# Performance work log

Measured on AMD Instinct MI355X. Metric: run time of the kernel, lower is better.

Reference implementation:

```python
import jax, jax.numpy as jnp
import numpy as np

L = 16            # num_levels
F = 2             # features per level
T = 1 << 19       # hashmap size
BASE = 16         # base resolution
RES = 512         # desired_resolution (outer trilinear grid)
N_PTS = 262144

# 8 corner offsets of a unit cube, [8,3]
OFFS = np.array([[(c >> 0) & 1, (c >> 1) & 1, (c >> 2) & 1] for c in range(8)], dtype=np.uint32)
OFFS_J = jnp.asarray(OFFS)
OFFS_B = jnp.asarray(OFFS.astype(bool))
P1 = jnp.uint32(2654435761)
P2 = jnp.uint32(805459861)


def hash_encode(x01, table):
    """Instant-NGP multiresolution hash encoding. x01: [N,3] in [0,1]. table: [L,T,F]."""
    feats = []
    for l in range(L):
        res = BASE * (2 ** l)
        pos = x01 * res                      # [N,3]
        p0 = jnp.floor(pos)
        frac = pos - p0                      # [N,3]
        corners = p0.astype(jnp.uint32)[:, None, :] + OFFS_J[None]   # [N,8,3]
        if (res + 1) ** 3 <= T:              # dense level
            c = jnp.minimum(corners, jnp.uint32(res))
            idx = c[..., 0] + c[..., 1] * jnp.uint32(res + 1) + c[..., 2] * jnp.uint32((res + 1) * (res + 1))
        else:                                # hashed level (spatial hash, xor of primes)
            idx = corners[..., 0] ^ (corners[..., 1] * P1) ^ (corners[..., 2] * P2)
            idx = idx & jnp.uint32(T - 1)
        g = table[l][idx.astype(jnp.int32)]  # [N,8,F]
        w = jnp.where(OFFS_B[None], frac[:, None, :], 1.0 - frac[:, None, :]).prod(-1)  # [N,8]
        feats.append(jnp.einsum('nc,ncf->nf', w, g))
    return jnp.concatenate(feats, axis=-1)   # [N, L*F]


def mlp(x, W0, W1, W2):
    h = jax.nn.relu(x @ W0)
    h = jax.nn.relu(h @ W1)
    return h @ W2


def setup_inputs() -> dict:
    key = jax.random.key(0)
    k1, k2, k3, k4, k5 = jax.random.split(key, 5)
    xyz = jax.random.uniform(k1, (N_PTS, 3), dtype=jnp.float32, minval=-1.0, maxval=1.0)
    table = jax.random.uniform(k2, (L, T, F), dtype=jnp.float32, minval=-1e-4, maxval=1e-4)
    W0 = jax.random.normal(k3, (L * F, 64), dtype=jnp.float32) * (1.0 / np.sqrt(L * F))
    W1 = jax.random.normal(k4, (64, 64), dtype=jnp.float32) * (1.0 / 8.0)
    W2 = jax.random.normal(k5, (64, 8), dtype=jnp.float32) * (1.0 / 8.0)
    return {"xyz": xyz, "table": table, "W0": W0, "W1": W1, "W2": W2, "bound": 1}


def reference(xyz, table, W0, W1, W2, bound):
    xn = (xyz + bound) / (2 * bound)          # [N,3] in [0,1]
    coords = xn * RES
    c0 = jnp.clip(jnp.floor(coords), 0.0, RES - 1.0)   # [N,3] floats holding ints
    frac = coords - c0                         # u,v,w per-axis [N,3]
    out = jnp.zeros((xyz.shape[0], 8), dtype=xyz.dtype)
    for b in range(8):
        bits = np.array([(b >> 0) & 1, (b >> 1) & 1, (b >> 2) & 1], dtype=np.float32)
        cc = (c0 + bits) / RES                 # corner point normalized to [0,1]
        f = mlp(hash_encode(cc, table), W0, W1, W2)   # [N,8]
        w = jnp.where(bits.astype(bool), frac, 1.0 - frac).prod(-1)  # [N]
        out = out + w[:, None] * f
    return out
```

## Files before the change

kernel.cpp:

```cpp
#include <hip/hip_runtime.h>


typedef __attribute__((ext_vector_type(8))) short short8_t;
typedef __attribute__((ext_vector_type(4))) float f32x4;

static constexpr unsigned kT    = 1u << 19;
static constexpr unsigned kMask = kT - 1u;
static constexpr unsigned cP1   = 2654435761u;
static constexpr unsigned cP2   = 805459861u;
static constexpr int      BLOCK = 256;
static constexpr int      TOFF  = 4096;
static constexpr unsigned DOFF  = 1u << 21;
static constexpr unsigned DN0   = 4913;
static constexpr unsigned DN1   = 40850;
static constexpr unsigned DENSE_N = 315475;
static constexpr unsigned PARTO = 2621440u;
static constexpr size_t   WS_NEED  = ((size_t)TOFF + (1u << 21)) * 4;
static constexpr size_t   WS_NEED2 = ((size_t)PARTO + (1u << 22)) * 4;

static __device__ __forceinline__ unsigned bf16_rn(float x) {
    unsigned u = __float_as_uint(x);
    return (u + 0x7fffu + ((u >> 16) & 1u)) >> 16;
}

static __device__ __forceinline__ float2 bf2dec(unsigned u) {
    return make_float2(__uint_as_float(u << 16),
                       __uint_as_float(u & 0xffff0000u));
}

static __device__ __forceinline__ unsigned cvtpk(float lo, float hi) {
    unsigned r;
    asm("v_cvt_pk_bf16_f32 %0, %1, %2" : "=v"(r) : "v"(lo), "v"(hi));
    return r;
}

static __device__ __forceinline__ f32x4 mfma16(short8_t a, short8_t b, f32x4 c) {
    return __builtin_amdgcn_mfma_f32_16x16x32_bf16(a, b, c, 0, 0, 0);
}

__global__ __launch_bounds__(256)
void prep_all(const float* __restrict__ W0, const float* __restrict__ W1,
              const float* __restrict__ W2, const float2* __restrict__ tbl,
              unsigned* __restrict__ ws, int ncc, int ncf, int ncd)
{
    const int bx = blockIdx.x, tid = threadIdx.x;
    if (bx < ncc) {
        const int i = bx * 256 + tid;
        const float4 v = ((const float4*)(tbl + (size_t)3 * kT))[i];
        ((uint2*)(ws + TOFF))[i] =
            make_uint2(bf16_rn(v.x) | (bf16_rn(v.y) << 16),
                       bf16_rn(v.z) | (bf16_rn(v.w) << 16));
    } else if (bx < ncc + ncf) {
        const int i = (bx - ncc) * 256 + tid;
        const unsigned vv = (1u << 20) - 1u - (unsigned)i;
        const int s = __clz((int)vv) - 12;
        const unsigned fo = (1u << 20) - ((1u << 20) >> s);
        const unsigned j = (unsigned)i - fo;
        const float2 e = tbl[((size_t)(5 + s) << 19) + ((size_t)j << s)];
        (ws + TOFF + (1u << 20))[i] = bf16_rn(e.x) | (bf16_rn(e.y) << 16);
    } else if (bx < ncc + ncf + ncd) {
        const int i = (bx - ncc - ncf) * 256 + tid;
        if (i < (int)DENSE_N) {
            int l, off;
            if (i < (int)DN0)      { l = 0; off = i; }
            else if (i < (int)DN1) { l = 1; off = i - (int)DN0; }
            else                   { l = 2; off = i - (int)DN1; }
            const float2 e = tbl[(size_t)l * kT + off];
            ws[TOFF + DOFF + i] = bf16_rn(e.x) | (bf16_rn(e.y) << 16);
        }
    } else {
        const int t = (bx - ncc - ncf - ncd) * 4 + (tid >> 6);
        if (t >= 14) return;
        const int lane = tid & 63;
        const int n = lane & 15, q = lane >> 4;
        unsigned hi[4];
        #pragma unroll
        for (int d = 0; d < 4; ++d) {
            unsigned h2[2];
            #pragma unroll
            for (int s = 0; s < 2; ++s) {
                const int j = d * 2 + s;
                float v;
                if (t < 4) {
                    v = W0[(q * 8 + j) * 64 + t * 16 + n];
                } else {
                    const int kp = (j < 4) ? (q * 4 + j) : (16 + q * 4 + (j - 4));
                    if (t < 12) v = W1[(((t - 4) & 1) * 32 + kp) * 64 + ((t - 4) >> 1) * 16 + n];
                    else        v = (n < 8) ? W2[((t - 12) * 32 + kp) * 8 + n] : 0.0f;
                }
                h2[s] = bf16_rn(v);
            }
            hi[d] = h2[0] | (h2[1] << 16);
        }
        ((uint4*)ws)[t * 64 + lane] = make_uint4(hi[0], hi[1], hi[2], hi[3]);
    }
}

__global__ __launch_bounds__(256, 8)
void ngp_pa(const float* __restrict__ xyz, const int* __restrict__ boundp,
            unsigned* __restrict__ ws)
{
    const int tid = threadIdx.x;
    const int ge  = blockIdx.x * 256 + tid;
    const int pt  = ge >> 3;
    const int b   = ge & 7;

    const float bnd = (float)boundp[0];
    const float sc  = 0.5f / bnd;
    const float cxf = (xyz[pt * 3 + 0] + bnd) * sc * 512.0f;
    const float cyf = (xyz[pt * 3 + 1] + bnd) * sc * 512.0f;
    const float czf = (xyz[pt * 3 + 2] + bnd) * sc * 512.0f;
    const float c0x = fminf(fmaxf(floorf(cxf), 0.0f), 511.0f);
    const float c0y = fminf(fmaxf(floorf(cyf), 0.0f), 511.0f);
    const float c0z = fminf(fmaxf(floorf(czf), 0.0f), 511.0f);
    const unsigned kx = (unsigned)c0x + (unsigned)(b & 1);
    const unsigned ky = (unsigned)c0y + (unsigned)((b >> 1) & 1);
    const unsigned kz = (unsigned)c0z + (unsigned)((b >> 2) & 1);

    const unsigned* __restrict__ tbx = ws + TOFF;
    unsigned gH[2][8];
    #pragma unroll
    for (int l = 3; l < 5; ++l) {
        const int d = 5 - l;
        const unsigned qx = kx >> d, qy = ky >> d, qz = kz >> d;
        const unsigned hy0 = qy * cP1, hy1 = hy0 + cP1;
        const unsigned hz0 = qz * cP2, hz1 = hz0 + cP2;
        const unsigned x1u = qx + 1u;
        unsigned hidx[8];
        hidx[0] = (qx  ^ hy0 ^ hz0) & kMask;  hidx[1] = (x1u ^ hy0 ^ hz0) & kMask;
        hidx[2] = (qx  ^ hy1 ^ hz0) & kMask;  hidx[3] = (x1u ^ hy1 ^ hz0) & kMask;
        hidx[4] = (qx  ^ hy0 ^ hz1) & kMask;  hidx[5] = (x1u ^ hy0 ^ hz1) & kMask;
        hidx[6] = (qx  ^ hy1 ^ hz1) & kMask;  hidx[7] = (x1u ^ hy1 ^ hz1) & kMask;
        const unsigned* __restrict__ base = tbx + (size_t)(l - 3) * kT;
        #pragma unroll
        for (int c = 0; c < 8; ++c) gH[l - 3][c] = base[hidx[c]];
    }

    unsigned xd34[2];
    #pragma unroll
    for (int l = 3; l < 5; ++l) {
        const int d = 5 - l;
        const unsigned m = (1u << d) - 1u;
        const float inv = 1.0f / (float)(1 << d);
        const float fx = (float)(kx & m) * inv;
        const float fy = (float)(ky & m) * inv;
        const float fz = (float)(kz & m) * inv;
        const float2 g0 = bf2dec(gH[l - 3][0]), g1 = bf2dec(gH[l - 3][1]);
        const float2 g2 = bf2dec(gH[l - 3][2]), g3 = bf2dec(gH[l - 3][3]);
        const float2 g4 = bf2dec(gH[l - 3][4]), g5 = bf2dec(gH[l - 3][5]);
        const float2 g6 = bf2dec(gH[l - 3][6]), g7 = bf2dec(gH[l - 3][7]);
        const float wx1 = fx, wx0 = 1.0f - fx;
        const float wy1 = fy, wy0 = 1.0f - fy;
        const float wz1 = fz, wz0 = 1.0f - fz;
        const float w00 = wx0 * wy0, w10 = wx1 * wy0, w01 = wx0 * wy1, w11 = wx1 * wy1;
        const float a0 = w00 * wz0, a1 = w10 * wz0, a2 = w01 * wz0, a3 = w11 * wz0;
        const float a4 = w00 * wz1, a5 = w10 * wz1, a6 = w01 * wz1, a7 = w11 * wz1;
        const float vx = a0 * g0.x + a1 * g1.x + a2 * g2.x + a3 * g3.x
                       + a4 * g4.x + a5 * g5.x + a6 * g6.x + a7 * g7.x;
        const float vy = a0 * g0.y + a1 * g1.y + a2 * g2.y + a3 * g3.y
                       + a4 * g4.y + a5 * g5.y + a6 * g6.y + a7 * g7.y;
        xd34[l - 3] = cvtpk(vx, vy);
    }
    ((uint2*)(ws + PARTO))[ge] = make_uint2(xd34[0], xd34[1]);
}

__global__ __launch_bounds__(BLOCK, 5)
void ngp_pb(const float*  __restrict__ xyz,
            const int*    __restrict__ boundp,
            const unsigned* __restrict__ wsw,
            float*        __restrict__ out)
{
    __shared__ __align__(16) unsigned lds[4096];
    const int tid  = threadIdx.x;
    const int lane = tid & 63;
    const int wv   = tid >> 6;
    const int col  = lane & 15;
    const int q    = lane >> 4;
    const int swz  = (tid ^ (tid >> 2) ^ (tid >> 4)) & 3;

    const unsigned* __restrict__ tbx = wsw + TOFF;
    const float bnd = (float)boundp[0];
    const float sc  = 0.5f / bnd;
    const f32x4 zero = {0.0f, 0.0f, 0.0f, 0.0f};

    const int ge = blockIdx.x * BLOCK + tid;
    const int pt = ge >> 3;
    const int b  = ge & 7;

    const float cxf = (xyz[pt * 3 + 0] + bnd) * sc * 512.0f;
    const float cyf = (xyz[pt * 3 + 1] + bnd) * sc * 512.0f;
    const float czf = (xyz[pt * 3 + 2] + bnd) * sc * 512.0f;
    const float c0x = fminf(fmaxf(floorf(cxf), 0.0f), 511.0f);
    const float c0y = fminf(fmaxf(floorf(cyf), 0.0f), 511.0f);
    const float c0z = fminf(fmaxf(floorf(czf), 0.0f), 511.0f);
    const float frx = cxf - c0x;
    const float fry = cyf - c0y;
    const float frz = czf - c0z;

    const unsigned kx = (unsigned)c0x + (unsigned)(b & 1);
    const unsigned ky = (unsigned)c0y + (unsigned)((b >> 1) & 1);
    const unsigned kz = (unsigned)c0z + (unsigned)((b >> 2) & 1);

    const float wb = ((b & 1) ? frx : 1.0f - frx)
                   * ((b & 2) ? fry : 1.0f - fry)
                   * ((b & 4) ? frz : 1.0f - frz);

    const unsigned kyp = ky * cP1;
    const unsigned kzp = kz * cP2;
    const unsigned X   = kx ^ kyp ^ kzp;
    unsigned gfu[11];
    #pragma unroll
    for (int l = 5; l < 16; ++l) {
        const int s = l - 5;
        const unsigned base = (1u << 20) + ((1u << 20) - ((1u << 20) >> s));
        gfu[l - 5] = tbx[base + (X & (kMask >> s))];
    }

    const uint2 p34 = ((const uint2*)(wsw + PARTO))[ge];

    unsigned xd[16];
    #pragma unroll
    for (int l = 0; l < 3; ++l) {
        const int d = 5 - l;
        const unsigned m = (1u << d) - 1u;
        const float inv = 1.0f / (float)(1 << d);
        const unsigned qx = kx >> d, qy = ky >> d, qz = kz >> d;
        const float fx = (float)(kx & m) * inv;
        const float fy = (float)(ky & m) * inv;
        const float fz = (float)(kz & m) * inv;
        const unsigned res = 16u << l;
        const unsigned R = res + 1u, R2 = R * R;
        const unsigned x0 = (qx < res ? qx : res);
        const unsigned x1 = (qx + 1u < res ? qx + 1u : res);
        const unsigned y0 = (qy < res ? qy : res) * R;
        const unsigned y1 = (qy + 1u < res ? qy + 1u : res) * R;
        const unsigned z0 = (qz < res ? qz : res) * R2;
        const unsigned z1 = (qz + 1u < res ? qz + 1u : res) * R2;
        const unsigned dbase = DOFF + (l == 0 ? 0u : (l == 1 ? DN0 : DN1));
        const unsigned* __restrict__ base = tbx + dbase;
        const float2 g0 = bf2dec(base[x0 + y0 + z0]), g1 = bf2dec(base[x1 + y0 + z0]);
        const float2 g2 = bf2dec(base[x0 + y1 + z0]), g3 = bf2dec(base[x1 + y1 + z0]);
        const float2 g4 = bf2dec(base[x0 + y0 + z1]), g5 = bf2dec(base[x1 + y0 + z1]);
        const float2 g6 = bf2dec(base[x0 + y1 + z1]), g7 = bf2dec(base[x1 + y1 + z1]);
        const float wx1 = fx, wx0 = 1.0f - fx;
        const float wy1 = fy, wy0 = 1.0f - fy;
        const float wz1 = fz, wz0 = 1.0f - fz;
        const float w00 = wx0 * wy0, w10 = wx1 * wy0, w01 = wx0 * wy1, w11 = wx1 * wy1;
        const float a0 = w00 * wz0, a1 = w10 * wz0, a2 = w01 * wz0, a3 = w11 * wz0;
        const float a4 = w00 * wz1, a5 = w10 * wz1, a6 = w01 * wz1, a7 = w11 * wz1;
        const float vx = a0 * g0.x + a1 * g1.x + a2 * g2.x + a3 * g3.x
                       + a4 * g4.x + a5 * g5.x + a6 * g6.x + a7 * g7.x;
        const float vy = a0 * g0.y + a1 * g1.y + a2 * g2.y + a3 * g3.y
                       + a4 * g4.y + a5 * g5.y + a6 * g6.y + a7 * g7.y;
        xd[l] = cvtpk(vx, vy);
    }
    xd[3] = p34.x;
    xd[4] = p34.y;
    #pragma unroll
    for (int l = 5; l < 16; ++l) xd[l] = gfu[l - 5];

    {
        uint4* xrow = (uint4*)(lds + tid * 16);
        xrow[swz]     = make_uint4(xd[0],  xd[1],  xd[2],  xd[3]);
        xrow[swz ^ 1] = make_uint4(xd[4],  xd[5],  xd[6],  xd[7]);
        xrow[swz ^ 2] = make_uint4(xd[8],  xd[9],  xd[10], xd[11]);
        xrow[swz ^ 3] = make_uint4(xd[12], xd[13], xd[14], xd[15]);
    }

    asm volatile("s_waitcnt lgkmcnt(0)" ::: "memory");
    __builtin_amdgcn_sched_barrier(0);

    short8_t w[14];
    {
        const short8_t* __restrict__ wfr = (const short8_t*)wsw;
        #pragma unroll
        for (int t = 0; t < 14; ++t) w[t] = wfr[t * 64 + lane];
    }

    #pragma unroll 1
    for (int g = 0; g < 4; ++g) {
        const int ev  = wv * 64 + g * 16 + col;
        const int esw = ((ev ^ (ev >> 2) ^ (ev >> 4)) & 3) ^ q;
        const short8_t xb = *(const short8_t*)(lds + ev * 16 + esw * 4);
        const float wbv = __shfl(wb, g * 16 + col, 64);

        unsigned hp0[4], hp1[4];
        #pragma unroll
        for (int mt = 0; mt < 4; ++mt) {
            f32x4 a = mfma16(w[mt], xb, zero);
            hp0[mt] = cvtpk(fmaxf(a[0], 0.0f), fmaxf(a[1], 0.0f));
            hp1[mt] = cvtpk(fmaxf(a[2], 0.0f), fmaxf(a[3], 0.0f));
        }
        uint4 u0 = make_uint4(hp0[0], hp1[0], hp0[1], hp1[1]);
        uint4 u1 = make_uint4(hp0[2], hp1[2], hp0[3], hp1[3]);
        short8_t bk0 = *(short8_t*)&u0;
        short8_t bk1 = *(short8_t*)&u1;

        #pragma unroll
        for (int mt = 0; mt < 4; ++mt) {
            f32x4 a = mfma16(w[4 + mt * 2], bk0, zero);
            a = mfma16(w[5 + mt * 2], bk1, a);
            hp0[mt] = cvtpk(fmaxf(a[0], 0.0f), fmaxf(a[1], 0.0f));
            hp1[mt] = cvtpk(fmaxf(a[2], 0.0f), fmaxf(a[3], 0.0f));
        }
        u0 = make_uint4(hp0[0], hp1[0], hp0[1], hp1[1]);
        u1 = make_uint4(hp0[2], hp1[2], hp0[3], hp1[3]);
        bk0 = *(short8_t*)&u0;
        bk1 = *(short8_t*)&u1;

        f32x4 a3 = mfma16(w[12], bk0, zero);
        a3 = mfma16(w[13], bk1, a3);

        float v0 = wbv * a3[0], v1 = wbv * a3[1], v2 = wbv * a3[2], v3 = wbv * a3[3];
        #pragma unroll
        for (int s = 1; s < 8; s <<= 1) {
            v0 += __shfl_xor(v0, s);
            v1 += __shfl_xor(v1, s);
            v2 += __shfl_xor(v2, s);
            v3 += __shfl_xor(v3, s);
        }
        if (((lane & 7) == 0) && q < 2) {
            const int p = (blockIdx.x * BLOCK + ev) >> 3;
            *(float4*)(out + p * 8 + q * 4) = make_float4(v0, v1, v2, v3);
        }
    }
}

template<bool BT>
__global__ __launch_bounds__(BLOCK, 5)
void ngp_mfma(const float*  __restrict__ xyz,
              const float2* __restrict__ tbl,
              const int*    __restrict__ boundp,
              const unsigned* __restrict__ wsw,
              float*        __restrict__ out,
              int ntiles)
{
    __shared__ __align__(16) unsigned lds[4096];
    const int tid  = threadIdx.x;
    const int lane = tid & 63;
    const int wv   = tid >> 6;
    const int col  = lane & 15;
    const int q    = lane >> 4;
    const int swz  = (tid ^ (tid >> 2) ^ (tid >> 4)) & 3;

    const unsigned* __restrict__ tbx = wsw + TOFF;
    const float bnd = (float)boundp[0];
    const float sc  = 0.5f / bnd;
    const f32x4 zero = {0.0f, 0.0f, 0.0f, 0.0f};

    const int ge = blockIdx.x * BLOCK + tid;
    const int pt = ge >> 3;
    const int b  = ge & 7;

    const float cxf = (xyz[pt * 3 + 0] + bnd) * sc * 512.0f;
    const float cyf = (xyz[pt * 3 + 1] + bnd) * sc * 512.0f;
    const float czf = (xyz[pt * 3 + 2] + bnd) * sc * 512.0f;
    const float c0x = fminf(fmaxf(floorf(cxf), 0.0f), 511.0f);
    const float c0y = fminf(fmaxf(floorf(cyf), 0.0f), 511.0f);
    const float c0z = fminf(fmaxf(floorf(czf), 0.0f), 511.0f);
    const float frx = cxf - c0x;
    const float fry = cyf - c0y;
    const float frz = czf - c0z;

    const unsigned kx = (unsigned)c0x + (unsigned)(b & 1);
    const unsigned ky = (unsigned)c0y + (unsigned)((b >> 1) & 1);
    const unsigned kz = (unsigned)c0z + (unsigned)((b >> 2) & 1);

    const float wb = ((b & 1) ? frx : 1.0f - frx)
                   * ((b & 2) ? fry : 1.0f - fry)
                   * ((b & 4) ? frz : 1.0f - frz);

    const unsigned kyp = ky * cP1;
    const unsigned kzp = kz * cP2;
    const unsigned X   = kx ^ kyp ^ kzp;
    unsigned gfu[11];
    float2   gff[11];
    #pragma unroll
    for (int l = 5; l < 16; ++l) {
        const int s = l - 5;
        if (BT) {
            const unsigned base = (1u << 20) + ((1u << 20) - ((1u << 20) >> s));
            gfu[l - 5] = tbx[base + (X & (kMask >> s))];
        } else {
            const unsigned idx = ((kx << s) ^ (kyp << s) ^ (kzp << s)) & kMask;
            gff[l - 5] = tbl[(size_t)l * kT + idx];
        }
    }

    unsigned gH[2][8];
    float2   gHf[2][8];
    #pragma unroll
    for (int l = 3; l < 5; ++l) {
        const int d = 5 - l;
        const unsigned qx = kx >> d, qy = ky >> d, qz = kz >> d;
        const unsigned hy0 = qy * cP1, hy1 = hy0 + cP1;
        const unsigned hz0 = qz * cP2, hz1 = hz0 + cP2;
        const unsigned x1u = qx + 1u;
        unsigned hidx[8];
        hidx[0] = (qx  ^ hy0 ^ hz0) & kMask;  hidx[1] = (x1u ^ hy0 ^ hz0) & kMask;
        hidx[2] = (qx  ^ hy1 ^ hz0) & kMask;  hidx[3] = (x1u ^ hy1 ^ hz0) & kMask;
        hidx[4] = (qx  ^ hy0 ^ hz1) & kMask;  hidx[5] = (x1u ^ hy0 ^ hz1) & kMask;
        hidx[6] = (qx  ^ hy1 ^ hz1) & kMask;  hidx[7] = (x1u ^ hy1 ^ hz1) & kMask;
        if (BT) {
            const unsigned* __restrict__ base = tbx + (size_t)(l - 3) * kT;
            #pragma unroll
            for (int c = 0; c < 8; ++c) gH[l - 3][c] = base[hidx[c]];
        } else {
            const float2* __restrict__ base = tbl + (size_t)l * kT;
            #pragma unroll
            for (int c = 0; c < 8; ++c) gHf[l - 3][c] = base[hidx[c]];
        }
    }

    float2 gc[5];
    #pragma unroll
    for (int l = 0; l < 5; ++l) {
        const int d = 5 - l;
        const unsigned m = (1u << d) - 1u;
        const float inv = 1.0f / (float)(1 << d);
        const unsigned qx = kx >> d, qy = ky >> d, qz = kz >> d;
        const float fx = (float)(kx & m) * inv;
        const float fy = (float)(ky & m) * inv;
        const float fz = (float)(kz & m) * inv;
        float2 g0, g1, g2, g3, g4, g5, g6, g7;
        if (l < 3) {
            const unsigned res = 16u << l;
            const unsigned R = res + 1u, R2 = R * R;
            const unsigned x0 = (qx < res ? qx : res);
            const unsigned x1 = (qx + 1u < res ? qx + 1u : res);
            const unsigned y0 = (qy < res ? qy : res) * R;
            const unsigned y1 = (qy + 1u < res ? qy + 1u : res) * R;
            const unsigned z0 = (qz < res ? qz : res) * R2;
            const unsigned z1 = (qz + 1u < res ? qz + 1u : res) * R2;
            const float2* __restrict__ base = tbl + (size_t)l * kT;
            g0 = base[x0 + y0 + z0]; g1 = base[x1 + y0 + z0];
            g2 = base[x0 + y1 + z0]; g3 = base[x1 + y1 + z0];
            g4 = base[x0 + y0 + z1]; g5 = base[x1 + y0 + z1];
            g6 = base[x0 + y1 + z1]; g7 = base[x1 + y1 + z1];
        } else if (BT) {
            g0 = bf2dec(gH[l - 3][0]); g1 = bf2dec(gH[l - 3][1]);
            g2 = bf2dec(gH[l - 3][2]); g3 = bf2dec(gH[l - 3][3]);
            g4 = bf2dec(gH[l - 3][4]); g5 = bf2dec(gH[l - 3][5]);
            g6 = bf2dec(gH[l - 3][6]); g7 = bf2dec(gH[l - 3][7]);
        } else {
            g0 = gHf[l - 3][0]; g1 = gHf[l - 3][1]; g2 = gHf[l - 3][2]; g3 = gHf[l - 3][3];
            g4 = gHf[l - 3][4]; g5 = gHf[l - 3][5]; g6 = gHf[l - 3][6]; g7 = gHf[l - 3][7];
        }
        const float wx1 = fx, wx0 = 1.0f - fx;
        const float wy1 = fy, wy0 = 1.0f - fy;
        const float wz1 = fz, wz0 = 1.0f - fz;
        const float w00 = wx0 * wy0, w10 = wx1 * wy0, w01 = wx0 * wy1, w11 = wx1 * wy1;
        const float a0 = w00 * wz0, a1 = w10 * wz0, a2 = w01 * wz0, a3 = w11 * wz0;
        const float a4 = w00 * wz1, a5 = w10 * wz1, a6 = w01 * wz1, a7 = w11 * wz1;
        float vx = a0 * g0.x + a1 * g1.x + a2 * g2.x + a3 * g3.x
                 + a4 * g4.x + a5 * g5.x + a6 * g6.x + a7 * g7.x;
        float vy = a0 * g0.y + a1 * g1.y + a2 * g2.y + a3 * g3.y
                 + a4 * g4.y + a5 * g5.y + a6 * g6.y + a7 * g7.y;
        gc[l] = make_float2(vx, vy);
    }

    unsigned xd[16];
    #pragma unroll
    for (int l = 0; l < 5; ++l)
        xd[l] = cvtpk(gc[l].x, gc[l].y);
    #pragma unroll
    for (int l = 5; l < 16; ++l) {
        if (BT) xd[l] = gfu[l - 5];
        else    xd[l] = cvtpk(gff[l - 5].x, gff[l - 5].y);
    }
    {
        uint4* xrow = (uint4*)(lds + tid * 16);
        xrow[swz]     = make_uint4(xd[0],  xd[1],  xd[2],  xd[3]);
        xrow[swz ^ 1] = make_uint4(xd[4],  xd[5],  xd[6],  xd[7]);
        xrow[swz ^ 2] = make_uint4(xd[8],  xd[9],  xd[10], xd[11]);
        xrow[swz ^ 3] = make_uint4(xd[12], xd[13], xd[14], xd[15]);
    }

    asm volatile("s_waitcnt lgkmcnt(0)" ::: "memory");
    __builtin_amdgcn_sched_barrier(0);

    short8_t w[14];
    {
        const short8_t* __restrict__ wfr = (const short8_t*)wsw;
        #pragma unroll
        for (int t = 0; t < 14; ++t) w[t] = wfr[t * 64 + lane];
    }

    #pragma unroll 1
    for (int g = 0; g < 4; ++g) {
        const int ev  = wv * 64 + g * 16 + col;
        const int esw = ((ev ^ (ev >> 2) ^ (ev >> 4)) & 3) ^ q;
        const short8_t xb = *(const short8_t*)(lds + ev * 16 + esw * 4);
        const float wbv = __shfl(wb, g * 16 + col, 64);

        unsigned hp0[4], hp1[4];
        #pragma unroll
        for (int mt = 0; mt < 4; ++mt) {
            f32x4 a = mfma16(w[mt], xb, zero);
            hp0[mt] = cvtpk(fmaxf(a[0], 0.0f), fmaxf(a[1], 0.0f));
            hp1[mt] = cvtpk(fmaxf(a[2], 0.0f), fmaxf(a[3], 0.0f));
        }
        uint4 u0 = make_uint4(hp0[0], hp1[0], hp0[1], hp1[1]);
        uint4 u1 = make_uint4(hp0[2], hp1[2], hp0[3], hp1[3]);
        short8_t bk0 = *(short8_t*)&u0;
        short8_t bk1 = *(short8_t*)&u1;

        #pragma unroll
        for (int mt = 0; mt < 4; ++mt) {
            f32x4 a = mfma16(w[4 + mt * 2], bk0, zero);
            a = mfma16(w[5 + mt * 2], bk1, a);
            hp0[mt] = cvtpk(fmaxf(a[0], 0.0f), fmaxf(a[1], 0.0f));
            hp1[mt] = cvtpk(fmaxf(a[2], 0.0f), fmaxf(a[3], 0.0f));
        }
        u0 = make_uint4(hp0[0], hp1[0], hp0[1], hp1[1]);
        u1 = make_uint4(hp0[2], hp1[2], hp0[3], hp1[3]);
        bk0 = *(short8_t*)&u0;
        bk1 = *(short8_t*)&u1;

        f32x4 a3 = mfma16(w[12], bk0, zero);
        a3 = mfma16(w[13], bk1, a3);

        float v0 = wbv * a3[0], v1 = wbv * a3[1], v2 = wbv * a3[2], v3 = wbv * a3[3];
        #pragma unroll
        for (int s = 1; s < 8; s <<= 1) {
            v0 += __shfl_xor(v0, s);
            v1 += __shfl_xor(v1, s);
            v2 += __shfl_xor(v2, s);
            v3 += __shfl_xor(v3, s);
        }
        if (((lane & 7) == 0) && q < 2) {
            const int p = (blockIdx.x * BLOCK + ev) >> 3;
            *(float4*)(out + p * 8 + q * 4) = make_float4(v0, v1, v2, v3);
        }
    }
}

extern "C" void kernel_launch(void* const* d_in, const int* in_sizes, int n_in,
                              void* d_out, int out_size, void* d_ws, size_t ws_size,
                              hipStream_t stream) {
    const float*  xyz = (const float*)d_in[0];
    const float2* tbl = (const float2*)d_in[1];
    const float*  W0  = (const float*)d_in[2];
    const float*  W1  = (const float*)d_in[3];
    const float*  W2  = (const float*)d_in[4];
    const int*    bnd = (const int*)d_in[5];
    float* out = (float*)d_out;

    const int npts   = in_sizes[0] / 3;
    const int total  = npts * 8;
    const int ntiles = total / BLOCK;

    const bool big2 = (ws_size >= WS_NEED2);
    const bool big  = (ws_size >= WS_NEED);
    const int ncc = big ? (1 << 19) / 256 : 0;
    const int ncf = big ? ((1 << 20) - (1 << 9)) / 256 : 0;
    const int ncd = big2 ? (int)((DENSE_N + 255) / 256) : 0;

    hipLaunchKernelGGL(prep_all, dim3(ncc + ncf + ncd + 4), dim3(256), 0, stream,
                       W0, W1, W2, tbl, (unsigned*)d_ws, ncc, ncf, ncd);

    if (big2) {
        hipLaunchKernelGGL(ngp_pa, dim3(total / 256), dim3(256), 0, stream,
                           xyz, bnd, (unsigned*)d_ws);
        hipLaunchKernelGGL(ngp_pb, dim3(ntiles), dim3(BLOCK), 0, stream,
                           xyz, bnd, (const unsigned*)d_ws, out);
    } else if (big) {
        hipLaunchKernelGGL(ngp_mfma<true>, dim3(ntiles), dim3(BLOCK), 0, stream,
                           xyz, tbl, bnd, (const unsigned*)d_ws, out, ntiles);
    } else {
        hipLaunchKernelGGL(ngp_mfma<false>, dim3(ntiles), dim3(BLOCK), 0, stream,
                           xyz, tbl, bnd, (const unsigned*)d_ws, out, ntiles);
    }
}
```

Before: 214.5 us.

## Fold dense levels 0-1 into one upsampled grid and use nontemporal memory ops

Precomputes level-0 features on the level-1 (33^3) grid. Every corner coordinate is even on the level-1 lattice, so the level-0 trilinear result can be stored next to the level-1 value in one 8-byte entry. Level 0 then needs no gathers of its own, cutting the dense-level gather count in the main kernel from 24 to 16. Separately, many table loads and stores switch to nontemporal builtins and ngp_pb's launch bound rises to 8 waves. This adds a prep pass with an extra rounding stage of level-0 features to bf16, and risks register spills at the higher occupancy target.

```diff
diff --git a/kernel.cpp b/kernel.cpp
--- a/kernel.cpp
+++ b/kernel.cpp
@@ -3,6 +3,7 @@
 
 typedef __attribute__((ext_vector_type(8))) short short8_t;
 typedef __attribute__((ext_vector_type(4))) float f32x4;
+typedef unsigned long long ull;
 
 static constexpr unsigned kT    = 1u << 19;
 static constexpr unsigned kMask = kT - 1u;
@@ -10,10 +11,10 @@
 static constexpr unsigned cP2   = 805459861u;
 static constexpr int      BLOCK = 256;
 static constexpr int      TOFF  = 4096;
-static constexpr unsigned DOFF  = 1u << 21;
-static constexpr unsigned DN0   = 4913;
-static constexpr unsigned DN1   = 40850;
-static constexpr unsigned DENSE_N = 315475;
+static constexpr unsigned D01   = 1u << 21;
+static constexpr unsigned N01   = 35937u;
+static constexpr unsigned D2    = D01 + 72000u;
+static constexpr unsigned N2    = 274625u;
 static constexpr unsigned PARTO = 2621440u;
 static constexpr size_t   WS_NEED  = ((size_t)TOFF + (1u << 21)) * 4;
 static constexpr size_t   WS_NEED2 = ((size_t)PARTO + (1u << 22)) * 4;
@@ -41,35 +42,74 @@
 __global__ __launch_bounds__(256)
 void prep_all(const float* __restrict__ W0, const float* __restrict__ W1,
               const float* __restrict__ W2, const float2* __restrict__ tbl,
-              unsigned* __restrict__ ws, int ncc, int ncf, int ncd)
+              unsigned* __restrict__ ws, int ncc, int ncf, int ncd, int nc01)
 {
     const int bx = blockIdx.x, tid = threadIdx.x;
     if (bx < ncc) {
         const int i = bx * 256 + tid;
-        const float4 v = ((const float4*)(tbl + (size_t)3 * kT))[i];
-        ((uint2*)(ws + TOFF))[i] =
-            make_uint2(bf16_rn(v.x) | (bf16_rn(v.y) << 16),
-                       bf16_rn(v.z) | (bf16_rn(v.w) << 16));
+        const ull* __restrict__ p = (const ull*)(tbl + (size_t)3 * kT);
+        const ull a = __builtin_nontemporal_load(p + 2 * (size_t)i);
+        const ull b = __builtin_nontemporal_load(p + 2 * (size_t)i + 1);
+        const ull o = (ull)(bf16_rn(__uint_as_float((unsigned)a))
+                          | (bf16_rn(__uint_as_float((unsigned)(a >> 32))) << 16))
+                    | ((ull)(bf16_rn(__uint_as_float((unsigned)b))
+                          | (bf16_rn(__uint_as_float((unsigned)(b >> 32))) << 16)) << 32);
+        __builtin_nontemporal_store(o, (ull*)(ws + TOFF) + i);
     } else if (bx < ncc + ncf) {
         const int i = (bx - ncc) * 256 + tid;
         const unsigned vv = (1u << 20) - 1u - (unsigned)i;
         const int s = __clz((int)vv) - 12;
         const unsigned fo = (1u << 20) - ((1u << 20) >> s);
         const unsigned j = (unsigned)i - fo;
-        const float2 e = tbl[((size_t)(5 + s) << 19) + ((size_t)j << s)];
-        (ws + TOFF + (1u << 20))[i] = bf16_rn(e.x) | (bf16_rn(e.y) << 16);
+        const ull e = __builtin_nontemporal_load(
+            (const ull*)tbl + ((size_t)(5 + s) << 19) + ((size_t)j << s));
+        const unsigned o = bf16_rn(__uint_as_float((unsigned)e))
+                         | (bf16_rn(__uint_as_float((unsigned)(e >> 32))) << 16);
+        __builtin_nontemporal_store(o, ws + TOFF + (1u << 20) + i);
     } else if (bx < ncc + ncf + ncd) {
         const int i = (bx - ncc - ncf) * 256 + tid;
-        if (i < (int)DENSE_N) {
-            int l, off;
-            if (i < (int)DN0)      { l = 0; off = i; }
-            else if (i < (int)DN1) { l = 1; off = i - (int)DN0; }
-            else                   { l = 2; off = i - (int)DN1; }
-            const float2 e = tbl[(size_t)l * kT + off];
-            ws[TOFF + DOFF + i] = bf16_rn(e.x) | (bf16_rn(e.y) << 16);
+        if (i < (int)N2) {
+            const ull e = __builtin_nontemporal_load(
+                (const ull*)tbl + (size_t)2 * kT + i);
+            const unsigned o = bf16_rn(__uint_as_float((unsigned)e))
+                             | (bf16_rn(__uint_as_float((unsigned)(e >> 32))) << 16);
+            __builtin_nontemporal_store(o, ws + TOFF + D2 + i);
+        }
+    } else if (bx < ncc + ncf + ncd + nc01) {
+        const int i = (bx - ncc - ncf - ncd) * 256 + tid;
+        if (i < (int)N01) {
+            const int vz = i / 1089;
+            const int r  = i - vz * 1089;
+            const int vy = r / 33;
+            const int vx = r - vy * 33;
+            const float2 f1 = tbl[(size_t)kT + i];
+            const int x0 = vx >> 1, y0 = vy >> 1, z0 = vz >> 1;
+            const int x1 = (x0 + 1 > 16) ? 16 : x0 + 1;
+            const int y1 = (y0 + 1 > 16) ? 16 : y0 + 1;
+            const int z1 = (z0 + 1 > 16) ? 16 : z0 + 1;
+            const float fx = (vx & 1) ? 0.5f : 0.0f;
+            const float fy = (vy & 1) ? 0.5f : 0.0f;
+            const float fz = (vz & 1) ? 0.5f : 0.0f;
+            const int Y0 = y0 * 17, Y1 = y1 * 17, Z0 = z0 * 289, Z1 = z1 * 289;
+            const float2 g0 = tbl[x0 + Y0 + Z0], g1 = tbl[x1 + Y0 + Z0];
+            const float2 g2 = tbl[x0 + Y1 + Z0], g3 = tbl[x1 + Y1 + Z0];
+            const float2 g4 = tbl[x0 + Y0 + Z1], g5 = tbl[x1 + Y0 + Z1];
+            const float2 g6 = tbl[x0 + Y1 + Z1], g7 = tbl[x1 + Y1 + Z1];
+            const float wx1 = fx, wx0 = 1.0f - fx;
+            const float wy1 = fy, wy0 = 1.0f - fy;
+            const float wz1 = fz, wz0 = 1.0f - fz;
+            const float w00 = wx0 * wy0, w10 = wx1 * wy0, w01 = wx0 * wy1, w11 = wx1 * wy1;
+            const float a0 = w00 * wz0, a1 = w10 * wz0, a2 = w01 * wz0, a3 = w11 * wz0;
+            const float a4 = w00 * wz1, a5 = w10 * wz1, a6 = w01 * wz1, a7 = w11 * wz1;
+            const float f0x = a0 * g0.x + a1 * g1.x + a2 * g2.x + a3 * g3.x
+                            + a4 * g4.x + a5 * g5.x + a6 * g6.x + a7 * g7.x;
+            const float f0y = a0 * g0.y + a1 * g1.y + a2 * g2.y + a3 * g3.y
+                            + a4 * g4.y + a5 * g5.y + a6 * g6.y + a7 * g7.y;
+            const ull o = (ull)cvtpk(f0x, f0y) | ((ull)cvtpk(f1.x, f1.y) << 32);
+            __builtin_nontemporal_store(o, (ull*)(ws + TOFF + D01) + i);
         }
     } else {
-        const int t = (bx - ncc - ncf - ncd) * 4 + (tid >> 6);
+        const int t = (bx - ncc - ncf - ncd - nc01) * 4 + (tid >> 6);
         if (t >= 14) return;
         const int lane = tid & 63;
         const int n = lane & 15, q = lane >> 4;
@@ -107,9 +147,12 @@
 
     const float bnd = (float)boundp[0];
     const float sc  = 0.5f / bnd;
-    const float cxf = (xyz[pt * 3 + 0] + bnd) * sc * 512.0f;
-    const float cyf = (xyz[pt * 3 + 1] + bnd) * sc * 512.0f;
-    const float czf = (xyz[pt * 3 + 2] + bnd) * sc * 512.0f;
+    const float pxv = __builtin_nontemporal_load(xyz + pt * 3 + 0);
+    const float pyv = __builtin_nontemporal_load(xyz + pt * 3 + 1);
+    const float pzv = __builtin_nontemporal_load(xyz + pt * 3 + 2);
+    const float cxf = (pxv + bnd) * sc * 512.0f;
+    const float cyf = (pyv + bnd) * sc * 512.0f;
+    const float czf = (pzv + bnd) * sc * 512.0f;
     const float c0x = fminf(fmaxf(floorf(cxf), 0.0f), 511.0f);
     const float c0y = fminf(fmaxf(floorf(cyf), 0.0f), 511.0f);
     const float c0z = fminf(fmaxf(floorf(czf), 0.0f), 511.0f);
@@ -161,10 +204,11 @@
                        + a4 * g4.y + a5 * g5.y + a6 * g6.y + a7 * g7.y;
         xd34[l - 3] = cvtpk(vx, vy);
     }
-    ((uint2*)(ws + PARTO))[ge] = make_uint2(xd34[0], xd34[1]);
-}
-
-__global__ __launch_bounds__(BLOCK, 5)
+    const ull o = (ull)xd34[0] | ((ull)xd34[1] << 32);
+    __builtin_nontemporal_store(o, (ull*)(ws + PARTO) + ge);
+}
+
+__global__ __launch_bounds__(BLOCK, 8)
 void ngp_pb(const float*  __restrict__ xyz,
             const int*    __restrict__ boundp,
             const unsigned* __restrict__ wsw,
@@ -187,9 +231,12 @@
     const int pt = ge >> 3;
     const int b  = ge & 7;
 
-    const float cxf = (xyz[pt * 3 + 0] + bnd) * sc * 512.0f;
-    const float cyf = (xyz[pt * 3 + 1] + bnd) * sc * 512.0f;
-    const float czf = (xyz[pt * 3 + 2] + bnd) * sc * 512.0f;
+    const float pxv = __builtin_nontemporal_load(xyz + pt * 3 + 0);
+    const float pyv = __builtin_nontemporal_load(xyz + pt * 3 + 1);
+    const float pzv = __builtin_nontemporal_load(xyz + pt * 3 + 2);
+    const float cxf = (pxv + bnd) * sc * 512.0f;
+    const float cyf = (pyv + bnd) * sc * 512.0f;
+    const float czf = (pzv + bnd) * sc * 512.0f;
     const float c0x = fminf(fmaxf(floorf(cxf), 0.0f), 511.0f);
     const float c0y = fminf(fmaxf(floorf(cyf), 0.0f), 511.0f);
     const float c0z = fminf(fmaxf(floorf(czf), 0.0f), 511.0f);
@@ -216,32 +263,62 @@
         gfu[l - 5] = tbx[base + (X & (kMask >> s))];
     }
 
-    const uint2 p34 = ((const uint2*)(wsw + PARTO))[ge];
+    const ull pv = __builtin_nontemporal_load((const ull*)(wsw + PARTO) + ge);
 
     unsigned xd[16];
-    #pragma unroll
-    for (int l = 0; l < 3; ++l) {
-        const int d = 5 - l;
-        const unsigned m = (1u << d) - 1u;
-        const float inv = 1.0f / (float)(1 << d);
-        const unsigned qx = kx >> d, qy = ky >> d, qz = kz >> d;
-        const float fx = (float)(kx & m) * inv;
-        const float fy = (float)(ky & m) * inv;
-        const float fz = (float)(kz & m) * inv;
-        const unsigned res = 16u << l;
-        const unsigned R = res + 1u, R2 = R * R;
-        const unsigned x0 = (qx < res ? qx : res);
-        const unsigned x1 = (qx + 1u < res ? qx + 1u : res);
-        const unsigned y0 = (qy < res ? qy : res) * R;
-        const unsigned y1 = (qy + 1u < res ? qy + 1u : res) * R;
-        const unsigned z0 = (qz < res ? qz : res) * R2;
-        const unsigned z1 = (qz + 1u < res ? qz + 1u : res) * R2;
-        const unsigned dbase = DOFF + (l == 0 ? 0u : (l == 1 ? DN0 : DN1));
-        const unsigned* __restrict__ base = tbx + dbase;
-        const float2 g0 = bf2dec(base[x0 + y0 + z0]), g1 = bf2dec(base[x1 + y0 + z0]);
-        const float2 g2 = bf2dec(base[x0 + y1 + z0]), g3 = bf2dec(base[x1 + y1 + z0]);
-        const float2 g4 = bf2dec(base[x0 + y0 + z1]), g5 = bf2dec(base[x1 + y0 + z1]);
-        const float2 g6 = bf2dec(base[x0 + y1 + z1]), g7 = bf2dec(base[x1 + y1 + z1]);
+    {
+        const unsigned qx = kx >> 4, qy = ky >> 4, qz = kz >> 4;
+        const float fx = (float)(kx & 15u) * 0.0625f;
+        const float fy = (float)(ky & 15u) * 0.0625f;
+        const float fz = (float)(kz & 15u) * 0.0625f;
+        const unsigned x0 = qx, x1 = (qx + 1u > 32u) ? 32u : qx + 1u;
+        const unsigned y0 = qy * 33u, y1 = ((qy + 1u > 32u) ? 32u : qy + 1u) * 33u;
+        const unsigned z0 = qz * 1089u, z1 = ((qz + 1u > 32u) ? 32u : qz + 1u) * 1089u;
+        const uint2* __restrict__ b01 = (const uint2*)(tbx + D01);
+        const uint2 h0 = b01[x0 + y0 + z0], h1 = b01[x1 + y0 + z0];
+        const uint2 h2 = b01[x0 + y1 + z0], h3 = b01[x1 + y1 + z0];
+        const uint2 h4 = b01[x0 + y0 + z1], h5 = b01[x1 + y0 + z1];
+        const uint2 h6 = b01[x0 + y1 + z1], h7 = b01[x1 + y1 + z1];
+        const float wx1 = fx, wx0 = 1.0f - fx;
+        const float wy1 = fy, wy0 = 1.0f - fy;
+        const float wz1 = fz, wz0 = 1.0f - fz;
+        const float w00 = wx0 * wy0, w10 = wx1 * wy0, w01 = wx0 * wy1, w11 = wx1 * wy1;
+        const float a0 = w00 * wz0, a1 = w10 * wz0, a2 = w01 * wz0, a3 = w11 * wz0;
+        const float a4 = w00 * wz1, a5 = w10 * wz1, a6 = w01 * wz1, a7 = w11 * wz1;
+        float f0x, f0y, f1x, f1y;
+        float2 d;
+        d = bf2dec(h0.x); f0x  = a0 * d.x; f0y  = a0 * d.y;
+        d = bf2dec(h0.y); f1x  = a0 * d.x; f1y  = a0 * d.y;
+        d = bf2dec(h1.x); f0x += a1 * d.x; f0y += a1 * d.y;
+        d = bf2dec(h1.y); f1x += a1 * d.x; f1y += a1 * d.y;
+        d = bf2dec(h2.x); f0x += a2 * d.x; f0y += a2 * d.y;
+        d = bf2dec(h2.y); f1x += a2 * d.x; f1y += a2 * d.y;
+        d = bf2dec(h3.x); f0x += a3 * d.x; f0y += a3 * d.y;
+        d = bf2dec(h3.y); f1x += a3 * d.x; f1y += a3 * d.y;
+        d = bf2dec(h4.x); f0x += a4 * d.x; f0y += a4 * d.y;
+        d = bf2dec(h4.y); f1x += a4 * d.x; f1y += a4 * d.y;
+        d = bf2dec(h5.x); f0x += a5 * d.x; f0y += a5 * d.y;
+        d = bf2dec(h5.y); f1x += a5 * d.x; f1y += a5 * d.y;
+        d = bf2dec(h6.x); f0x += a6 * d.x; f0y += a6 * d.y;
+        d = bf2dec(h6.y); f1x += a6 * d.x; f1y += a6 * d.y;
+        d = bf2dec(h7.x); f0x += a7 * d.x; f0y += a7 * d.y;
+        d = bf2dec(h7.y); f1x += a7 * d.x; f1y += a7 * d.y;
+        xd[0] = cvtpk(f0x, f0y);
+        xd[1] = cvtpk(f1x, f1y);
+    }
+    {
+        const unsigned qx = kx >> 3, qy = ky >> 3, qz = kz >> 3;
+        const float fx = (float)(kx & 7u) * 0.125f;
+        const float fy = (float)(ky & 7u) * 0.125f;
+        const float fz = (float)(kz & 7u) * 0.125f;
+        const unsigned x0 = qx, x1 = (qx + 1u > 64u) ? 64u : qx + 1u;
+        const unsigned y0 = qy * 65u, y1 = ((qy + 1u > 64u) ? 64u : qy + 1u) * 65u;
+        const unsigned z0 = qz * 4225u, z1 = ((qz + 1u > 64u) ? 64u : qz + 1u) * 4225u;
+        const unsigned* __restrict__ b2 = tbx + D2;
+        const float2 g0 = bf2dec(b2[x0 + y0 + z0]), g1 = bf2dec(b2[x1 + y0 + z0]);
+        const float2 g2 = bf2dec(b2[x0 + y1 + z0]), g3 = bf2dec(b2[x1 + y1 + z0]);
+        const float2 g4 = bf2dec(b2[x0 + y0 + z1]), g5 = bf2dec(b2[x1 + y0 + z1]);
+        const float2 g6 = bf2dec(b2[x0 + y1 + z1]), g7 = bf2dec(b2[x1 + y1 + z1]);
         const float wx1 = fx, wx0 = 1.0f - fx;
         const float wy1 = fy, wy0 = 1.0f - fy;
         const float wz1 = fz, wz0 = 1.0f - fz;
@@ -252,10 +329,10 @@
                        + a4 * g4.x + a5 * g5.x + a6 * g6.x + a7 * g7.x;
         const float vy = a0 * g0.y + a1 * g1.y + a2 * g2.y + a3 * g3.y
                        + a4 * g4.y + a5 * g5.y + a6 * g6.y + a7 * g7.y;
-        xd[l] = cvtpk(vx, vy);
-    }
-    xd[3] = p34.x;
-    xd[4] = p34.y;
+        xd[2] = cvtpk(vx, vy);
+    }
+    xd[3] = (unsigned)pv;
+    xd[4] = (unsigned)(pv >> 32);
     #pragma unroll
     for (int l = 5; l < 16; ++l) xd[l] = gfu[l - 5];
 
@@ -321,7 +398,11 @@
         }
         if (((lane & 7) == 0) && q < 2) {
             const int p = (blockIdx.x * BLOCK + ev) >> 3;
-            *(float4*)(out + p * 8 + q * 4) = make_float4(v0, v1, v2, v3);
+            ull* op = (ull*)(out + p * 8 + q * 4);
+            __builtin_nontemporal_store(
+                (ull)__float_as_uint(v0) | ((ull)__float_as_uint(v1) << 32), op);
+            __builtin_nontemporal_store(
+                (ull)__float_as_uint(v2) | ((ull)__float_as_uint(v3) << 32), op + 1);
         }
     }
 }
@@ -552,12 +633,14 @@
 
     const bool big2 = (ws_size >= WS_NEED2);
     const bool big  = (ws_size >= WS_NEED);
-    const int ncc = big ? (1 << 19) / 256 : 0;
-    const int ncf = big ? ((1 << 20) - (1 << 9)) / 256 : 0;
-    const int ncd = big2 ? (int)((DENSE_N + 255) / 256) : 0;
-
-    hipLaunchKernelGGL(prep_all, dim3(ncc + ncf + ncd + 4), dim3(256), 0, stream,
-                       W0, W1, W2, tbl, (unsigned*)d_ws, ncc, ncf, ncd);
+    const int ncc  = big ? (1 << 19) / 256 : 0;
+    const int ncf  = big ? ((1 << 20) - (1 << 9)) / 256 : 0;
+    const int ncd  = big2 ? (int)((N2 + 255u) / 256u) : 0;
+    const int nc01 = big2 ? (int)((N01 + 255u) / 256u) : 0;
+
+    hipLaunchKernelGGL(prep_all, dim3(ncc + ncf + ncd + nc01 + 4), dim3(256),
+                       0, stream, W0, W1, W2, tbl, (unsigned*)d_ws,
+                       ncc, ncf, ncd, nc01);
 
     if (big2) {
         hipLaunchKernelGGL(ngp_pa, dim3(total / 256), dim3(256), 0, stream,
```

Result: slower. 330.9 us (+54.3%).
